# Kernel optimization log

Measured on AMD Instinct MI355X. Metric: run time of the kernel, lower is better.

The kernel has to match this reference:

```python
import jax, jax.numpy as jnp
import numpy as np

B, T, L = 64, 256, 64          # batch, time steps, num_links
H = 128                        # hidden_size
E = 524288                     # num edges
N = B * T                      # nodes seen by GCNConv
IN = L + L * L                 # 4160: concat of link features + flattened distance matrix
OUT = 12 * L                   # fc output size
NUM_LSTM = 2


def setup_inputs() -> dict:
    key = jax.random.key(0)
    ks = jax.random.split(key, 24)
    inp = {
        "x": jax.random.normal(ks[0], (B, T, L), jnp.float32),
        "distance": jax.random.uniform(ks[1], (L, L), jnp.float32),
        "edge_index": jax.random.randint(ks[2], (2, E), 0, N, jnp.int64),
    }
    # GCN layer params (PyG GCNConv: lin weight [in,out] acting as x @ W, bias after aggregation)
    dims = [IN, H, H, H]
    for i in range(3):
        s = 1.0 / np.sqrt(dims[i])
        inp[f"gcn_W{i}"] = jax.random.normal(ks[3 + 2 * i], (dims[i], H), jnp.float32) * s
        inp[f"gcn_b{i}"] = jnp.zeros((H,), jnp.float32)
    # LSTM params, torch layout: W_ih [4H, Hin], W_hh [4H, H], gate order i,f,g,o
    s = 1.0 / np.sqrt(H)
    for l in range(NUM_LSTM):
        inp[f"Wih{l}"] = jax.random.normal(ks[10 + 4 * l], (4 * H, H), jnp.float32) * s
        inp[f"Whh{l}"] = jax.random.normal(ks[11 + 4 * l], (4 * H, H), jnp.float32) * s
        inp[f"bih{l}"] = jax.random.normal(ks[12 + 4 * l], (4 * H,), jnp.float32) * s
        inp[f"bhh{l}"] = jax.random.normal(ks[13 + 4 * l], (4 * H,), jnp.float32) * s
    inp["fc_W"] = jax.random.normal(ks[20], (OUT, H), jnp.float32) * s
    inp["fc_b"] = jnp.zeros((OUT,), jnp.float32)
    return inp


def _gcn(x, W, b, src, dst):
    # GCNConv with add_self_loops=True: out = D^-1/2 (A+I) D^-1/2 (x W) + b
    h = x @ W
    deg = jnp.ones((N,), h.dtype).at[dst].add(1.0)  # in-degree + self loop
    dinv = jax.lax.rsqrt(deg)
    norm = dinv[src] * dinv[dst]                    # [E]
    agg = jnp.zeros_like(h).at[dst].add(h[src] * norm[:, None])
    agg = agg + h * (dinv * dinv)[:, None]          # self-loop term
    return agg + b


def _lstm_layer(xs, Wih, Whh, bih, bhh):
    # xs: [T, B, Hin]
    bias = bih + bhh

    def step(carry, xt):
        h, c = carry
        g = xt @ Wih.T + h @ Whh.T + bias
        i, f, gg, o = jnp.split(g, 4, axis=-1)
        c = jax.nn.sigmoid(f) * c + jax.nn.sigmoid(i) * jnp.tanh(gg)
        h = jax.nn.sigmoid(o) * jnp.tanh(c)
        return (h, c), h

    h0 = jnp.zeros((xs.shape[1], H), xs.dtype)
    _, ys = jax.lax.scan(step, (h0, h0), xs)
    return ys


def reference(x, distance, gcn_W0, gcn_b0, gcn_W1, gcn_b1, gcn_W2, gcn_b2,
              Wih0, Whh0, bih0, bhh0, Wih1, Whh1, bih1, bhh1, fc_W, fc_b,
              edge_index):
    src, dst = edge_index[0], edge_index[1]
    xf = x.reshape(N, L)
    dist_flat = jnp.broadcast_to(distance.reshape(1, L * L), (N, L * L))
    feat = jnp.concatenate([xf, dist_flat], axis=1)  # [N, IN]
    for W, b in ((gcn_W0, gcn_b0), (gcn_W1, gcn_b1), (gcn_W2, gcn_b2)):
        feat = jax.nn.relu(_gcn(feat, W, b, src, dst))
    seq = feat.reshape(B, T, H).transpose(1, 0, 2)   # [T, B, H]
    seq = _lstm_layer(seq, Wih0, Whh0, bih0, bhh0)
    seq = _lstm_layer(seq, Wih1, Whh1, bih1, bhh1)
    last = seq[-1]                                   # [B, H]
    out = last @ fc_W.T + fc_b                       # [B, OUT]
    return out.reshape(B, 12, L)
```

## Files before the change

kernel.cpp:

```cpp
#include <hip/hip_runtime.h>
#include <hip/hip_bf16.h>
#include <cstdint>
#include <cstddef>

#define NB 64
#define NT 256
#define NL 64
#define NH 128
#define NN 16384
#define NE 524288
#define NG 512
#define NOUT 768

__device__ __forceinline__ unsigned rne_bf16(float f) {
  unsigned u = __float_as_uint(f);
  return (u + 0x7FFFu + ((u >> 16) & 1u)) >> 16;
}


__global__ __launch_bounds__(256) void k_transpose(const float* __restrict__ W,
                                                   float* __restrict__ Wt,
                                                   int K, int Nout) {
  int i = blockIdx.x * 256 + threadIdx.x;
  if (i < K * Nout) {
    int k = i / Nout, n = i % Nout;
    Wt[n * K + k] = W[i];
  }
}

__global__ __launch_bounds__(256) void k_dvec(const float* __restrict__ dist,
                                              const float* __restrict__ W0,
                                              float* __restrict__ dvec) {
  __shared__ float red[256];
  int j = blockIdx.x;
  int t = threadIdx.x;
  float acc = 0.f;
  for (int m = t; m < 4096; m += 256)
    acc += dist[m] * W0[(size_t)(64 + m) * 128 + j];
  red[t] = acc;
  __syncthreads();
  for (int off = 128; off > 0; off >>= 1) {
    if (t < off) red[t] += red[t + off];
    __syncthreads();
  }
  if (t == 0) dvec[j] = red[0];
}

__global__ __launch_bounds__(256) void k_count(const int* __restrict__ dst,
                                               int* __restrict__ counts) {
  int i = blockIdx.x * 256 + threadIdx.x;
  atomicAdd(&counts[dst[i]], 1);
}

__global__ __launch_bounds__(1024) void k_scan(const int* __restrict__ counts,
                                               int* __restrict__ rowstart,
                                               float* __restrict__ dinv) {
  __shared__ int part[1024];
  int t = threadIdx.x;
  int base = t * 16;
  int local[16];
  int s = 0;
#pragma unroll
  for (int i = 0; i < 16; i++) {
    int cv = counts[base + i];
    local[i] = s; s += cv;
    dinv[base + i] = rsqrtf((float)cv + 1.0f);
  }
  part[t] = s;
  __syncthreads();
  for (int off = 1; off < 1024; off <<= 1) {
    int v = (t >= off) ? part[t - off] : 0;
    __syncthreads();
    part[t] += v;
    __syncthreads();
  }
  int prefix = (t == 0) ? 0 : part[t - 1];
#pragma unroll
  for (int i = 0; i < 16; i++) rowstart[base + i] = prefix + local[i];
  if (t == 1023) rowstart[16384] = part[1023];
}

__global__ __launch_bounds__(256) void k_fill(const int* __restrict__ src,
                                              const int* __restrict__ dst,
                                              const int* __restrict__ rowstart,
                                              int* __restrict__ fill,
                                              const float* __restrict__ dinv,
                                              int2* __restrict__ csr) {
  int e = blockIdx.x * 256 + threadIdx.x;
  int sN = src[e], dN = dst[e];
  int pos = rowstart[dN] + atomicAdd(&fill[dN], 1);
  csr[pos] = make_int2(sN, __float_as_int(dinv[sN] * dinv[dN]));
}

template <int K, bool RELU, bool PERMC = false, bool OBF16 = false>
__global__ __launch_bounds__(256) void k_gemm_abt(const float* __restrict__ A,
                                                  const float* __restrict__ Bm,
                                                  const float* __restrict__ bias0,
                                                  const float* __restrict__ bias1,
                                                  void* __restrict__ Cv, int Nn) {
  __shared__ float As[64][K];
  __shared__ float Bs[64][K];
  const int tid = threadIdx.x;
  const int bm = blockIdx.x, bn = blockIdx.y;
  const int VPR = K / 4;
  for (int i = tid; i < 64 * VPR; i += 256) {
    int r = i / VPR, c = i % VPR;
    int xr = (r >> 2) & 7;
    float4 q = *(const float4*)(A + (size_t)(bm * 64 + r) * K + c * 4);
    *(float4*)&As[r][(c ^ xr) * 4] = q;
  }
  for (int i = tid; i < 64 * VPR; i += 256) {
    int r = i / VPR, c = i % VPR;
    int xr = (r >> 2) & 7;
    float4 q = *(const float4*)(Bm + (size_t)(bn * 64 + r) * K + c * 4);
    *(float4*)&Bs[r][(c ^ xr) * 4] = q;
  }
  __syncthreads();
  const int tr = (tid >> 4) << 2;
  const int tc = (tid & 15) << 2;
  const int axor = (tr >> 2) & 7;
  const int bxor = (tc >> 2) & 7;
  float acc[4][4] = {};
#pragma unroll 2
  for (int k4 = 0; k4 < VPR; k4++) {
    int ka = (k4 ^ axor) * 4;
    int kb = (k4 ^ bxor) * 4;
    float4 a0 = *(const float4*)&As[tr + 0][ka];
    float4 a1 = *(const float4*)&As[tr + 1][ka];
    float4 a2 = *(const float4*)&As[tr + 2][ka];
    float4 a3 = *(const float4*)&As[tr + 3][ka];
    float4 b0 = *(const float4*)&Bs[tc + 0][kb];
    float4 b1 = *(const float4*)&Bs[tc + 1][kb];
    float4 b2 = *(const float4*)&Bs[tc + 2][kb];
    float4 b3 = *(const float4*)&Bs[tc + 3][kb];
#define DOT4(i2, j2, av, bv)                                                   \
    acc[i2][j2] = fmaf(av.x, bv.x, acc[i2][j2]);                               \
    acc[i2][j2] = fmaf(av.y, bv.y, acc[i2][j2]);                               \
    acc[i2][j2] = fmaf(av.z, bv.z, acc[i2][j2]);                               \
    acc[i2][j2] = fmaf(av.w, bv.w, acc[i2][j2]);
    DOT4(0, 0, a0, b0) DOT4(0, 1, a0, b1) DOT4(0, 2, a0, b2) DOT4(0, 3, a0, b3)
    DOT4(1, 0, a1, b0) DOT4(1, 1, a1, b1) DOT4(1, 2, a1, b2) DOT4(1, 3, a1, b3)
    DOT4(2, 0, a2, b0) DOT4(2, 1, a2, b1) DOT4(2, 2, a2, b2) DOT4(2, 3, a2, b3)
    DOT4(3, 0, a3, b0) DOT4(3, 1, a3, b1) DOT4(3, 2, a3, b2) DOT4(3, 3, a3, b3)
#undef DOT4
  }
  const int col0 = bn * 64 + tc;
#pragma unroll
  for (int i2 = 0; i2 < 4; i2++) {
    int row = bm * 64 + tr + i2;
    float v[4];
#pragma unroll
    for (int j2 = 0; j2 < 4; j2++) {
      int col = col0 + j2;
      float t = acc[i2][j2];
      if (bias0) t += bias0[col];
      if (bias1) t += bias1[col];
      if (RELU) t = fmaxf(t, 0.f);
      v[j2] = t;
    }
    if (OBF16) {
      unsigned short* C = (unsigned short*)Cv;
      uint2 pk;
      pk.x = rne_bf16(v[0]) | (rne_bf16(v[1]) << 16);
      pk.y = rne_bf16(v[2]) | (rne_bf16(v[3]) << 16);
      *(uint2*)(C + (size_t)row * Nn + col0) = pk;
    } else {
      float* C = (float*)Cv;
#pragma unroll
      for (int j2 = 0; j2 < 4; j2++) {
        int col = col0 + j2;
        int colw = PERMC ? ((col & 127) * 4 + (col >> 7)) : col;
        C[(size_t)row * Nn + colw] = v[j2];
      }
    }
  }
}

typedef float f2v __attribute__((ext_vector_type(2)));
__device__ __forceinline__ f2v unpk2(unsigned d) {
  f2v r;
  r.x = __uint_as_float(d << 16);
  r.y = __uint_as_float(d & 0xFFFF0000u);
  return r;
}

__global__ __launch_bounds__(256) void k_agg(const unsigned* __restrict__ h,
                                             const int* __restrict__ rowstart,
                                             const int2* __restrict__ csr,
                                             const float* __restrict__ dinv,
                                             const float* __restrict__ bias,
                                             float* __restrict__ out) {
  int node = blockIdx.x * 4 + (threadIdx.x >> 6);
  int lane = threadIdx.x & 63;
  int s = rowstart[node], e = rowstart[node + 1];
  float ax = 0.f, ay = 0.f;
  int p = s;
  for (; p + 3 < e; p += 4) {
    int2 pk0 = csr[p];
    int2 pk1 = csr[p + 1];
    int2 pk2 = csr[p + 2];
    int2 pk3 = csr[p + 3];
    f2v hv0 = unpk2(h[(size_t)pk0.x * 64 + lane]);
    f2v hv1 = unpk2(h[(size_t)pk1.x * 64 + lane]);
    f2v hv2 = unpk2(h[(size_t)pk2.x * 64 + lane]);
    f2v hv3 = unpk2(h[(size_t)pk3.x * 64 + lane]);
    float w0 = __int_as_float(pk0.y);
    float w1 = __int_as_float(pk1.y);
    float w2 = __int_as_float(pk2.y);
    float w3 = __int_as_float(pk3.y);
    ax = fmaf(hv0.x, w0, ax); ay = fmaf(hv0.y, w0, ay);
    ax = fmaf(hv1.x, w1, ax); ay = fmaf(hv1.y, w1, ay);
    ax = fmaf(hv2.x, w2, ax); ay = fmaf(hv2.y, w2, ay);
    ax = fmaf(hv3.x, w3, ax); ay = fmaf(hv3.y, w3, ay);
  }
  for (; p < e; p++) {
    int2 pk0 = csr[p];
    f2v hv0 = unpk2(h[(size_t)pk0.x * 64 + lane]);
    float w0 = __int_as_float(pk0.y);
    ax = fmaf(hv0.x, w0, ax); ay = fmaf(hv0.y, w0, ay);
  }
  float di = dinv[node];
  float sw = di * di;
  f2v hs = unpk2(h[(size_t)node * 64 + lane]);
  float2 bv = ((const float2*)bias)[lane];
  ax = fmaf(hs.x, sw, ax) + bv.x;
  ay = fmaf(hs.y, sw, ay) + bv.y;
  float2 o;
  o.x = fmaxf(ax, 0.f);
  o.y = fmaxf(ay, 0.f);
  ((float2*)out)[(size_t)node * 64 + lane] = o;
}


template <int CTRL>
__device__ __forceinline__ float dppadd(float x) {
  int r = __builtin_amdgcn_update_dpp(0, __float_as_int(x), CTRL, 0xF, 0xF, true);
  return x + __int_as_float(r);
}

__device__ __forceinline__ float sigf(float x) {
  return 1.f / (1.f + __expf(-x));
}
__device__ __forceinline__ float tanhf_fast(float x) {
  return 1.f - 2.f / (__expf(2.f * x) + 1.f);
}

typedef float f4v __attribute__((ext_vector_type(4)));

template <bool LAST_ONLY>
__global__ __launch_bounds__(512)
__attribute__((amdgpu_waves_per_eu(2, 2)))
void k_lstm7(const float* __restrict__ pre,
             const float* __restrict__ Whh,
             float* __restrict__ yout) {
  __shared__ float hbuf[2][128];
  const int tid = threadIdx.x;
  const int b = blockIdx.x;
  const int c4 = tid & 3;
  const int u = tid >> 2;

  int hidx[8];
#pragma unroll
  for (int j = 0; j < 8; j++) hidx[j] = c4 * 8 + (((u & 7) + 2 * c4 + j) & 7);

#define DECLW(g, j) \
  f4v W##g##_##j = *(const f4v*)(Whh + (size_t)((g)*128 + u) * 128 + hidx[j] * 4);
#define DECLW_ROW(g) \
  DECLW(g, 0) DECLW(g, 1) DECLW(g, 2) DECLW(g, 3) \
  DECLW(g, 4) DECLW(g, 5) DECLW(g, 6) DECLW(g, 7)
  DECLW_ROW(0) DECLW_ROW(1) DECLW_ROW(2) DECLW_ROW(3)
#undef DECLW_ROW
#undef DECLW

  if (tid < 128) hbuf[0][tid] = 0.f;
  float cs = 0.f;
  const float* preb = pre + (size_t)b * NT * NG + tid;
  float pcur = preb[0];
  float* ybase = LAST_ONLY ? (yout + (size_t)b * NH + u)
                           : (yout + (size_t)b * NT * NH + u);
  __syncthreads();

#define PINW(g) \
  asm volatile("" : "+v"(W##g##_0), "+v"(W##g##_1), "+v"(W##g##_2), "+v"(W##g##_3)); \
  asm volatile("" : "+v"(W##g##_4), "+v"(W##g##_5), "+v"(W##g##_6), "+v"(W##g##_7));

#define FMA_J(j)                                                               \
  {                                                                            \
    f4v hv = hp[hidx[j]];                                                      \
    a0 = __builtin_elementwise_fma(W0_##j, hv, a0);                            \
    a1 = __builtin_elementwise_fma(W1_##j, hv, a1);                            \
    a2 = __builtin_elementwise_fma(W2_##j, hv, a2);                            \
    a3 = __builtin_elementwise_fma(W3_##j, hv, a3);                            \
  }

#define LSTM_STEP(CUR, NXT, T)                                                 \
  {                                                                            \
    int tn = (T) + 1; if (tn > NT - 1) tn = NT - 1;                            \
    float pnext = preb[(size_t)tn * NG];                                       \
    const f4v* hp = (const f4v*)&hbuf[CUR][0];                                 \
    f4v a0 = {0.f, 0.f, 0.f, 0.f}, a1 = a0, a2 = a0, a3 = a0;                  \
    FMA_J(0) FMA_J(1) FMA_J(2) FMA_J(3)                                        \
    FMA_J(4) FMA_J(5) FMA_J(6) FMA_J(7)                                        \
    float s0 = (a0.x + a0.y) + (a0.z + a0.w) + ((c4 == 0) ? pcur : 0.f);       \
    float s1 = (a1.x + a1.y) + (a1.z + a1.w) + ((c4 == 1) ? pcur : 0.f);       \
    float s2 = (a2.x + a2.y) + (a2.z + a2.w) + ((c4 == 2) ? pcur : 0.f);       \
    float s3 = (a3.x + a3.y) + (a3.z + a3.w) + ((c4 == 3) ? pcur : 0.f);       \
    s0 = dppadd<0xB1>(s0); s0 = dppadd<0x4E>(s0);                              \
    s1 = dppadd<0xB1>(s1); s1 = dppadd<0x4E>(s1);                              \
    s2 = dppadd<0xB1>(s2); s2 = dppadd<0x4E>(s2);                              \
    s3 = dppadd<0xB1>(s3); s3 = dppadd<0x4E>(s3);                              \
    float si = sigf(s0), sf = sigf(s1), tg = tanhf_fast(s2), so = sigf(s3);    \
    cs = sf * cs + si * tg;                                                    \
    float hnew = so * tanhf_fast(cs);                                          \
    if (c4 == 0) hbuf[NXT][u] = hnew;                                          \
    if (!LAST_ONLY) {                                                          \
      if (c4 == 1) ybase[(size_t)(T) * NH] = hnew;                             \
    } else if ((T) == NT - 1) {                                                \
      if (c4 == 1) *ybase = hnew;                                              \
    }                                                                          \
    pcur = pnext;                                                              \
    __syncthreads();                                                           \
  }

  for (int t = 0; t < NT; t += 2) {
    PINW(0) PINW(1) PINW(2) PINW(3)
    LSTM_STEP(0, 1, t);
    LSTM_STEP(1, 0, t + 1);
  }
#undef LSTM_STEP
#undef FMA_J
#undef PINW
}


extern "C" void kernel_launch(void* const* d_in, const int* in_sizes, int n_in,
                              void* d_out, int out_size, void* d_ws, size_t ws_size,
                              hipStream_t stream) {
  const float* x    = (const float*)d_in[0];
  const float* dist = (const float*)d_in[1];
  const int*   ei   = (const int*)d_in[2];
  const float* W0   = (const float*)d_in[3];
  const float* b0   = (const float*)d_in[4];
  const float* W1   = (const float*)d_in[5];
  const float* b1   = (const float*)d_in[6];
  const float* W2   = (const float*)d_in[7];
  const float* b2   = (const float*)d_in[8];
  const float* Wih0 = (const float*)d_in[9];
  const float* Whh0 = (const float*)d_in[10];
  const float* bih0 = (const float*)d_in[11];
  const float* bhh0 = (const float*)d_in[12];
  const float* Wih1 = (const float*)d_in[13];
  const float* Whh1 = (const float*)d_in[14];
  const float* bih1 = (const float*)d_in[15];
  const float* bhh1 = (const float*)d_in[16];
  const float* fcW  = (const float*)d_in[17];
  const float* fcb  = (const float*)d_in[18];
  float* out = (float*)d_out;

  char* ws = (char*)d_ws;
  size_t off = 0;
  auto alloc = [&](size_t bytes) -> void* {
    void* p = ws + off;
    off += (bytes + 255) & ~(size_t)255;
    return p;
  };
  float*    bufA     = (float*)alloc((size_t)NN * 128 * 4);
  float*    bufB     = (float*)alloc((size_t)NN * 128 * 4);
  unsigned short* h16 = (unsigned short*)alloc((size_t)NN * 128 * 2);
  float*    pre      = (float*)alloc((size_t)NN * 512 * 4);
  int2*     csr      = (int2*)alloc((size_t)NE * 8);
  int*      counts   = (int*)alloc((size_t)NN * 4);
  int*      fillc    = (int*)alloc((size_t)NN * 4);
  int*      rowstart = (int*)alloc((size_t)(NN + 1) * 4);
  float*    dinv     = (float*)alloc((size_t)NN * 4);
  float*    dvec     = (float*)alloc(128 * 4);
  float*    hlast    = (float*)alloc(64 * 128 * 4);
  float*    wt0      = (float*)alloc(128 * 64 * 4);
  float*    wt1      = (float*)alloc(128 * 128 * 4);
  float*    wt2      = (float*)alloc(128 * 128 * 4);
  (void)ws_size; (void)in_sizes; (void)n_in; (void)out_size;

  const int* srcIdx = ei;
  const int* dstIdx = ei + NE;

  hipMemsetAsync(counts, 0, (size_t)NN * 4, stream);
  hipMemsetAsync(fillc, 0, (size_t)NN * 4, stream);

  k_transpose<<<(64 * 128 + 255) / 256, 256, 0, stream>>>(W0, wt0, 64, 128);
  k_transpose<<<(128 * 128 + 255) / 256, 256, 0, stream>>>(W1, wt1, 128, 128);
  k_transpose<<<(128 * 128 + 255) / 256, 256, 0, stream>>>(W2, wt2, 128, 128);
  k_dvec<<<128, 256, 0, stream>>>(dist, W0, dvec);

  k_count<<<NE / 256, 256, 0, stream>>>(dstIdx, counts);
  k_scan<<<1, 1024, 0, stream>>>(counts, rowstart, dinv);
  k_fill<<<NE / 256, 256, 0, stream>>>(srcIdx, dstIdx, rowstart, fillc, dinv, csr);

  dim3 gH(NN / 64, 128 / 64);
  k_gemm_abt<64, false, false, true><<<gH, 256, 0, stream>>>(x, wt0, dvec, nullptr, h16, 128);
  k_agg<<<NN / 4, 256, 0, stream>>>((const unsigned*)h16, rowstart, csr, dinv, b0, bufA);
  k_gemm_abt<128, false, false, true><<<gH, 256, 0, stream>>>(bufA, wt1, nullptr, nullptr, h16, 128);
  k_agg<<<NN / 4, 256, 0, stream>>>((const unsigned*)h16, rowstart, csr, dinv, b1, bufA);
  k_gemm_abt<128, false, false, true><<<gH, 256, 0, stream>>>(bufA, wt2, nullptr, nullptr, h16, 128);
  k_agg<<<NN / 4, 256, 0, stream>>>((const unsigned*)h16, rowstart, csr, dinv, b2, bufA);

  dim3 gP(NN / 64, 512 / 64);
  k_gemm_abt<128, false, true><<<gP, 256, 0, stream>>>(bufA, Wih0, bih0, bhh0, pre, 512);
  k_lstm7<false><<<64, 512, 0, stream>>>(pre, Whh0, bufB);
  k_gemm_abt<128, false, true><<<gP, 256, 0, stream>>>(bufB, Wih1, bih1, bhh1, pre, 512);
  k_lstm7<true><<<64, 512, 0, stream>>>(pre, Whh1, hlast);

  dim3 gF(1, NOUT / 64);
  k_gemm_abt<128, false><<<gF, 256, 0, stream>>>(hlast, fcW, fcb, nullptr, out, NOUT);
}
```

Before: 756.5 us.

## Store LSTM recurrent weights as packed bf16 registers and use packed FMA

Adds a prepass that converts each Whh to bf16 and packs it into a per-thread swizzled uint4 layout, so the LSTM kernel holds half as many weight registers. The recurrent matvec now uses two-wide packed FMAs with bf16 unpacking instead of four-wide fp32 FMAs. The aim is lower register pressure and fewer instructions on the serial recurrence critical path. The cost is reduced precision in the recurrent weights, which compounds over 256 steps, plus unpack shift/mask ops and two extra small launches.

```diff
diff --git a/kernel.cpp b/kernel.cpp
--- a/kernel.cpp
+++ b/kernel.cpp
@@ -90,6 +90,25 @@
   int sN = src[e], dN = dst[e];
   int pos = rowstart[dN] + atomicAdd(&fill[dN], 1);
   csr[pos] = make_int2(sN, __float_as_int(dinv[sN] * dinv[dN]));
+}
+
+__global__ __launch_bounds__(256) void k_packw(const float* __restrict__ Whh,
+                                               uint4* __restrict__ out) {
+  int idx = blockIdx.x * 256 + threadIdx.x;
+  int c = idx >> 9, tid = idx & 511;
+  int u = tid >> 2, c4 = tid & 3;
+  int g = c >> 2, q = c & 3;
+  int h0 = c4 * 8 + (((u & 7) + 2 * c4 + 2 * q) & 7);
+  int h1 = c4 * 8 + (((u & 7) + 2 * c4 + 2 * q + 1) & 7);
+  const float* row = Whh + (size_t)(g * 128 + u) * 128;
+  const float* p0 = row + h0 * 4;
+  const float* p1 = row + h1 * 4;
+  uint4 o;
+  o.x = rne_bf16(p0[0]) | (rne_bf16(p0[1]) << 16);
+  o.y = rne_bf16(p0[2]) | (rne_bf16(p0[3]) << 16);
+  o.z = rne_bf16(p1[0]) | (rne_bf16(p1[1]) << 16);
+  o.w = rne_bf16(p1[2]) | (rne_bf16(p1[3]) << 16);
+  out[c * 512 + tid] = o;
 }
 
 template <int K, bool RELU, bool PERMC = false, bool OBF16 = false>
@@ -183,6 +202,9 @@
   r.y = __uint_as_float(d & 0xFFFF0000u);
   return r;
 }
+__device__ __forceinline__ f2v mk2(float a, float b) {
+  f2v r; r.x = a; r.y = b; return r;
+}
 
 __global__ __launch_bounds__(256) void k_agg(const unsigned* __restrict__ h,
                                              const int* __restrict__ rowstart,
@@ -246,13 +268,14 @@
 }
 
 typedef float f4v __attribute__((ext_vector_type(4)));
+typedef unsigned u4v __attribute__((ext_vector_type(4)));
 
 template <bool LAST_ONLY>
 __global__ __launch_bounds__(512)
 __attribute__((amdgpu_waves_per_eu(2, 2)))
-void k_lstm7(const float* __restrict__ pre,
-             const float* __restrict__ Whh,
-             float* __restrict__ yout) {
+void k_lstm8n(const float* __restrict__ pre,
+              const uint4* __restrict__ wpk,
+              float* __restrict__ yout) {
   __shared__ float hbuf[2][128];
   const int tid = threadIdx.x;
   const int b = blockIdx.x;
@@ -263,14 +286,13 @@
 #pragma unroll
   for (int j = 0; j < 8; j++) hidx[j] = c4 * 8 + (((u & 7) + 2 * c4 + j) & 7);
 
-#define DECLW(g, j) \
-  f4v W##g##_##j = *(const f4v*)(Whh + (size_t)((g)*128 + u) * 128 + hidx[j] * 4);
-#define DECLW_ROW(g) \
-  DECLW(g, 0) DECLW(g, 1) DECLW(g, 2) DECLW(g, 3) \
-  DECLW(g, 4) DECLW(g, 5) DECLW(g, 6) DECLW(g, 7)
-  DECLW_ROW(0) DECLW_ROW(1) DECLW_ROW(2) DECLW_ROW(3)
-#undef DECLW_ROW
-#undef DECLW
+  const u4v* wq = (const u4v*)wpk;
+#define DECLQ(g, q) u4v Q##g##_##q = wq[((g) * 4 + (q)) * 512 + tid];
+  DECLQ(0, 0) DECLQ(0, 1) DECLQ(0, 2) DECLQ(0, 3)
+  DECLQ(1, 0) DECLQ(1, 1) DECLQ(1, 2) DECLQ(1, 3)
+  DECLQ(2, 0) DECLQ(2, 1) DECLQ(2, 2) DECLQ(2, 3)
+  DECLQ(3, 0) DECLQ(3, 1) DECLQ(3, 2) DECLQ(3, 3)
+#undef DECLQ
 
   if (tid < 128) hbuf[0][tid] = 0.f;
   float cs = 0.f;
@@ -280,17 +302,29 @@
                            : (yout + (size_t)b * NT * NH + u);
   __syncthreads();
 
-#define PINW(g) \
-  asm volatile("" : "+v"(W##g##_0), "+v"(W##g##_1), "+v"(W##g##_2), "+v"(W##g##_3)); \
-  asm volatile("" : "+v"(W##g##_4), "+v"(W##g##_5), "+v"(W##g##_6), "+v"(W##g##_7));
-
-#define FMA_J(j)                                                               \
+#define PINQ(g) \
+  asm volatile("" : "+v"(Q##g##_0), "+v"(Q##g##_1), "+v"(Q##g##_2), "+v"(Q##g##_3));
+
+#define GATEN(g, SG)                                                           \
   {                                                                            \
-    f4v hv = hp[hidx[j]];                                                      \
-    a0 = __builtin_elementwise_fma(W0_##j, hv, a0);                            \
-    a1 = __builtin_elementwise_fma(W1_##j, hv, a1);                            \
-    a2 = __builtin_elementwise_fma(W2_##j, hv, a2);                            \
-    a3 = __builtin_elementwise_fma(W3_##j, hv, a3);                            \
+    f2v ag = {0.f, 0.f};                                                       \
+    ag = __builtin_elementwise_fma(unpk2(Q##g##_0.x), mk2(h0.x, h0.y), ag);    \
+    ag = __builtin_elementwise_fma(unpk2(Q##g##_0.y), mk2(h0.z, h0.w), ag);    \
+    ag = __builtin_elementwise_fma(unpk2(Q##g##_0.z), mk2(h1.x, h1.y), ag);    \
+    ag = __builtin_elementwise_fma(unpk2(Q##g##_0.w), mk2(h1.z, h1.w), ag);    \
+    ag = __builtin_elementwise_fma(unpk2(Q##g##_1.x), mk2(h2.x, h2.y), ag);    \
+    ag = __builtin_elementwise_fma(unpk2(Q##g##_1.y), mk2(h2.z, h2.w), ag);    \
+    ag = __builtin_elementwise_fma(unpk2(Q##g##_1.z), mk2(h3.x, h3.y), ag);    \
+    ag = __builtin_elementwise_fma(unpk2(Q##g##_1.w), mk2(h3.z, h3.w), ag);    \
+    ag = __builtin_elementwise_fma(unpk2(Q##g##_2.x), mk2(h4.x, h4.y), ag);    \
+    ag = __builtin_elementwise_fma(unpk2(Q##g##_2.y), mk2(h4.z, h4.w), ag);    \
+    ag = __builtin_elementwise_fma(unpk2(Q##g##_2.z), mk2(h5.x, h5.y), ag);    \
+    ag = __builtin_elementwise_fma(unpk2(Q##g##_2.w), mk2(h5.z, h5.w), ag);    \
+    ag = __builtin_elementwise_fma(unpk2(Q##g##_3.x), mk2(h6.x, h6.y), ag);    \
+    ag = __builtin_elementwise_fma(unpk2(Q##g##_3.y), mk2(h6.z, h6.w), ag);    \
+    ag = __builtin_elementwise_fma(unpk2(Q##g##_3.z), mk2(h7.x, h7.y), ag);    \
+    ag = __builtin_elementwise_fma(unpk2(Q##g##_3.w), mk2(h7.z, h7.w), ag);    \
+    SG = ag.x + ag.y;                                                          \
   }
 
 #define LSTM_STEP(CUR, NXT, T)                                                 \
@@ -298,13 +332,14 @@
     int tn = (T) + 1; if (tn > NT - 1) tn = NT - 1;                            \
     float pnext = preb[(size_t)tn * NG];                                       \
     const f4v* hp = (const f4v*)&hbuf[CUR][0];                                 \
-    f4v a0 = {0.f, 0.f, 0.f, 0.f}, a1 = a0, a2 = a0, a3 = a0;                  \
-    FMA_J(0) FMA_J(1) FMA_J(2) FMA_J(3)                                        \
-    FMA_J(4) FMA_J(5) FMA_J(6) FMA_J(7)                                        \
-    float s0 = (a0.x + a0.y) + (a0.z + a0.w) + ((c4 == 0) ? pcur : 0.f);       \
-    float s1 = (a1.x + a1.y) + (a1.z + a1.w) + ((c4 == 1) ? pcur : 0.f);       \
-    float s2 = (a2.x + a2.y) + (a2.z + a2.w) + ((c4 == 2) ? pcur : 0.f);       \
-    float s3 = (a3.x + a3.y) + (a3.z + a3.w) + ((c4 == 3) ? pcur : 0.f);       \
+    f4v h0 = hp[hidx[0]], h1 = hp[hidx[1]], h2 = hp[hidx[2]], h3 = hp[hidx[3]];\
+    f4v h4 = hp[hidx[4]], h5 = hp[hidx[5]], h6 = hp[hidx[6]], h7 = hp[hidx[7]];\
+    float s0, s1, s2, s3;                                                      \
+    GATEN(0, s0) GATEN(1, s1) GATEN(2, s2) GATEN(3, s3)                        \
+    s0 += (c4 == 0) ? pcur : 0.f;                                              \
+    s1 += (c4 == 1) ? pcur : 0.f;                                              \
+    s2 += (c4 == 2) ? pcur : 0.f;                                              \
+    s3 += (c4 == 3) ? pcur : 0.f;                                              \
     s0 = dppadd<0xB1>(s0); s0 = dppadd<0x4E>(s0);                              \
     s1 = dppadd<0xB1>(s1); s1 = dppadd<0x4E>(s1);                              \
     s2 = dppadd<0xB1>(s2); s2 = dppadd<0x4E>(s2);                              \
@@ -323,13 +358,13 @@
   }
 
   for (int t = 0; t < NT; t += 2) {
-    PINW(0) PINW(1) PINW(2) PINW(3)
+    PINQ(0) PINQ(1) PINQ(2) PINQ(3)
     LSTM_STEP(0, 1, t);
     LSTM_STEP(1, 0, t + 1);
   }
 #undef LSTM_STEP
-#undef FMA_J
-#undef PINW
+#undef GATEN
+#undef PINQ
 }
 
 
@@ -378,6 +413,8 @@
   float*    wt0      = (float*)alloc(128 * 64 * 4);
   float*    wt1      = (float*)alloc(128 * 128 * 4);
   float*    wt2      = (float*)alloc(128 * 128 * 4);
+  uint4*    wpk0     = (uint4*)alloc((size_t)8192 * 16);
+  uint4*    wpk1     = (uint4*)alloc((size_t)8192 * 16);
   (void)ws_size; (void)in_sizes; (void)n_in; (void)out_size;
 
   const int* srcIdx = ei;
@@ -390,6 +427,8 @@
   k_transpose<<<(128 * 128 + 255) / 256, 256, 0, stream>>>(W1, wt1, 128, 128);
   k_transpose<<<(128 * 128 + 255) / 256, 256, 0, stream>>>(W2, wt2, 128, 128);
   k_dvec<<<128, 256, 0, stream>>>(dist, W0, dvec);
+  k_packw<<<32, 256, 0, stream>>>(Whh0, wpk0);
+  k_packw<<<32, 256, 0, stream>>>(Whh1, wpk1);
 
   k_count<<<NE / 256, 256, 0, stream>>>(dstIdx, counts);
   k_scan<<<1, 1024, 0, stream>>>(counts, rowstart, dinv);
@@ -405,9 +444,9 @@
 
   dim3 gP(NN / 64, 512 / 64);
   k_gemm_abt<128, false, true><<<gP, 256, 0, stream>>>(bufA, Wih0, bih0, bhh0, pre, 512);
-  k_lstm7<false><<<64, 512, 0, stream>>>(pre, Whh0, bufB);
+  k_lstm8n<false><<<64, 512, 0, stream>>>(pre, wpk0, bufB);
   k_gemm_abt<128, false, true><<<gP, 256, 0, stream>>>(bufB, Wih1, bih1, bhh1, pre, 512);
-  k_lstm7<true><<<64, 512, 0, stream>>>(pre, Whh1, hlast);
+  k_lstm8n<true><<<64, 512, 0, stream>>>(pre, wpk1, hlast);
 
   dim3 gF(1, NOUT / 64);
   k_gemm_abt<128, false><<<gF, 256, 0, stream>>>(hlast, fcW, fcb, nullptr, out, NOUT);
```

Result: slower. 834.8 us (+10.4%).
